# Kernel tuning notes

Measured on AMD Instinct MI355X. Metric: run time of the kernel, lower is better.

The kernel has to match this reference:

```python
import jax, jax.numpy as jnp
import numpy as np

B = 1024
N = 100  # graph_size
D = 128


def setup_inputs() -> dict:
    key = jax.random.key(0)
    k1, k2 = jax.random.split(key)
    x = jax.random.normal(k1, (B * N, D), dtype=jnp.float32)
    edge_index = jax.random.randint(k2, (2, B * N * (N - 1)), 0, N, dtype=jnp.int64)
    return {"x": x, "edge_index": edge_index, "graph_size": N}


def reference(x, edge_index, graph_size):
    # x: [B*N, D] -> [B, N, D]; edge_index is split but never used in the math.
    b = x.shape[0] // graph_size
    xb = x.reshape(b, graph_size, -1)
    # per-graph dot-product logits: [B, N, N]
    logits = jnp.einsum('bnd,bmd->bnm', xb, xb)
    # segment softmax with index j = column index of the flattened [N*N] logits:
    # normalizes over rows i for each column j -> softmax along axis=1.
    return jax.nn.softmax(logits, axis=1)
```

## Files before the change

### kernel.cpp

```cpp
#include <hip/hip_runtime.h>

#define NG 100
#define DD 128

#define REDMAX 6400
#define REDSUM 6800
#define SMSZ   7200

__global__ __launch_bounds__(256, 4)
void dotdec_kernel(const float* __restrict__ x, float* __restrict__ out) {
    __shared__ float sm[SMSZ];
    const int t    = threadIdx.x;
    const int lane = t & 63;
    const int wave = t >> 6;
    const int b    = blockIdx.x;
    const float* xb = x   + (size_t)b * (NG * DD);
    float*       ob = out + (size_t)b * (NG * NG);

    float acc[7][4][2];
#pragma unroll
    for (int i = 0; i < 7; ++i)
#pragma unroll
        for (int j = 0; j < 4; ++j) { acc[i][j][0] = 0.f; acc[i][j][1] = 0.f; }

    for (int h = 0; h < 2; ++h) {
        if (h) __syncthreads();
#pragma unroll
        for (int k = 0; k < 7; ++k) {
            int i4 = t + 256 * k;
            if (i4 < 1600) {
                int n  = i4 >> 4;
                int dq = i4 & 15;
                float4 v = ((const float4*)xb)[n * 32 + h * 16 + dq];
                int dl = dq * 4;
                sm[(dl + 0) * NG + n] = v.x;
                sm[(dl + 1) * NG + n] = v.y;
                sm[(dl + 2) * NG + n] = v.z;
                sm[(dl + 3) * NG + n] = v.w;
            }
        }
        __syncthreads();

        for (int dl = 0; dl < 64; ++dl) {
            const float* row = &sm[dl * NG];
            float2 mv = *(const float2*)&row[2 * lane];
#pragma unroll
            for (int i = 0; i < 6; ++i) {
                int nt = wave + 4 * i;
                float4 nv = *(const float4*)&row[4 * nt];
                acc[i][0][0] += nv.x * mv.x; acc[i][0][1] += nv.x * mv.y;
                acc[i][1][0] += nv.y * mv.x; acc[i][1][1] += nv.y * mv.y;
                acc[i][2][0] += nv.z * mv.x; acc[i][2][1] += nv.z * mv.y;
                acc[i][3][0] += nv.w * mv.x; acc[i][3][1] += nv.w * mv.y;
            }
            if (wave == 0) {
                float4 nv = *(const float4*)&row[96];
                acc[6][0][0] += nv.x * mv.x; acc[6][0][1] += nv.x * mv.y;
                acc[6][1][0] += nv.y * mv.x; acc[6][1][1] += nv.y * mv.y;
                acc[6][2][0] += nv.z * mv.x; acc[6][2][1] += nv.z * mv.y;
                acc[6][3][0] += nv.w * mv.x; acc[6][3][1] += nv.w * mv.y;
            }
        }
    }

    float px0 = -3.402823466e38f, px1 = -3.402823466e38f;
#pragma unroll
    for (int i = 0; i < 6; ++i)
#pragma unroll
        for (int j = 0; j < 4; ++j) {
            px0 = fmaxf(px0, acc[i][j][0]);
            px1 = fmaxf(px1, acc[i][j][1]);
        }
    if (wave == 0)
#pragma unroll
        for (int j = 0; j < 4; ++j) {
            px0 = fmaxf(px0, acc[6][j][0]);
            px1 = fmaxf(px1, acc[6][j][1]);
        }

    __syncthreads();
    if (lane < 50)
        *(float2*)&sm[REDMAX + wave * NG + 2 * lane] = make_float2(px0, px1);
    __syncthreads();

    float2 q0 = *(const float2*)&sm[REDMAX + 0   + 2 * lane];
    float2 q1 = *(const float2*)&sm[REDMAX + 100 + 2 * lane];
    float2 q2 = *(const float2*)&sm[REDMAX + 200 + 2 * lane];
    float2 q3 = *(const float2*)&sm[REDMAX + 300 + 2 * lane];
    float gx0 = fmaxf(fmaxf(q0.x, q1.x), fmaxf(q2.x, q3.x));
    float gx1 = fmaxf(fmaxf(q0.y, q1.y), fmaxf(q2.y, q3.y));

    float ps0 = 0.f, ps1 = 0.f;
#pragma unroll
    for (int i = 0; i < 6; ++i)
#pragma unroll
        for (int j = 0; j < 4; ++j) {
            float e0 = __expf(acc[i][j][0] - gx0); acc[i][j][0] = e0; ps0 += e0;
            float e1 = __expf(acc[i][j][1] - gx1); acc[i][j][1] = e1; ps1 += e1;
        }
    if (wave == 0)
#pragma unroll
        for (int j = 0; j < 4; ++j) {
            float e0 = __expf(acc[6][j][0] - gx0); acc[6][j][0] = e0; ps0 += e0;
            float e1 = __expf(acc[6][j][1] - gx1); acc[6][j][1] = e1; ps1 += e1;
        }
    if (lane < 50)
        *(float2*)&sm[REDSUM + wave * NG + 2 * lane] = make_float2(ps0, ps1);
    __syncthreads();

    float2 u0 = *(const float2*)&sm[REDSUM + 0   + 2 * lane];
    float2 u1 = *(const float2*)&sm[REDSUM + 100 + 2 * lane];
    float2 u2 = *(const float2*)&sm[REDSUM + 200 + 2 * lane];
    float2 u3 = *(const float2*)&sm[REDSUM + 300 + 2 * lane];

    if (lane < 50) {
        float r0 = 1.f / ((u0.x + u1.x) + (u2.x + u3.x));
        float r1 = 1.f / ((u0.y + u1.y) + (u2.y + u3.y));
#pragma unroll
        for (int i = 0; i < 6; ++i) {
            int nt = wave + 4 * i;
#pragma unroll
            for (int j = 0; j < 4; ++j) {
                int n = 4 * nt + j;
                *(float2*)&ob[n * NG + 2 * lane] =
                    make_float2(acc[i][j][0] * r0, acc[i][j][1] * r1);
            }
        }
        if (wave == 0)
#pragma unroll
            for (int j = 0; j < 4; ++j) {
                int n = 96 + j;
                *(float2*)&ob[n * NG + 2 * lane] =
                    make_float2(acc[6][j][0] * r0, acc[6][j][1] * r1);
            }
    }
}

extern "C" void kernel_launch(void* const* d_in, const int* in_sizes, int n_in,
                              void* d_out, int out_size, void* d_ws, size_t ws_size,
                              hipStream_t stream) {
    const float* x = (const float*)d_in[0];
    float* out = (float*)d_out;
    const int B = in_sizes[0] / (NG * DD);
    dim3 grid(B), block(256);
    hipLaunchKernelGGL(dotdec_kernel, grid, block, 0, stream, x, out);
}
```

Baseline: 189.4 us.

## Compute per-graph Gram matrix with bf16 MFMA and wave-local softmax reduction

Replaces the fp32 scalar FMA outer-product loop with 16x16x32 bf16 MFMA instructions. Inputs are converted to bf16 in LDS with a padded row stride, and each wave owns one or two 16-column tiles. Because a wave now holds whole columns, the column softmax max and sum reductions use lane shuffles instead of LDS round trips and block barriers. The bf16 rounding lowers the precision of the logits, which softmax can amplify, and the output stores become scalar rather than float2.

```diff
diff --git a/kernel.cpp b/kernel.cpp
--- a/kernel.cpp
+++ b/kernel.cpp
@@ -2,138 +2,123 @@
 
 #define NG 100
 #define DD 128
+#define NPAD 112
+#define LSTRIDE 136
 
-#define REDMAX 6400
-#define REDSUM 6800
-#define SMSZ   7200
+typedef __attribute__((ext_vector_type(8))) short bf16x8;
+typedef __attribute__((ext_vector_type(4))) float floatx4;
+
+__device__ __forceinline__ unsigned int f2bf(float f) {
+    unsigned int u = __float_as_uint(f);
+    return (u + 0x7FFFu + ((u >> 16) & 1u)) >> 16;
+}
 
 __global__ __launch_bounds__(256, 4)
-void dotdec_kernel(const float* __restrict__ x, float* __restrict__ out) {
-    __shared__ float sm[SMSZ];
+void dotdec_mfma(const float* __restrict__ x, float* __restrict__ out) {
+    __shared__ unsigned short xs[NPAD * LSTRIDE];
     const int t    = threadIdx.x;
     const int lane = t & 63;
     const int wave = t >> 6;
-    const int b    = blockIdx.x;
-    const float* xb = x   + (size_t)b * (NG * DD);
-    float*       ob = out + (size_t)b * (NG * NG);
+    const int quad = lane >> 4;
+    const int lr   = lane & 15;
+    const size_t b = blockIdx.x;
+    const float* xb = x   + b * (size_t)(NG * DD);
+    float*       ob = out + b * (size_t)(NG * NG);
 
-    float acc[7][4][2];
+    for (int i = t; i < 12 * 64; i += 256) {
+        int r = 100 + (i >> 6), cp = i & 63;
+        *(unsigned int*)&xs[r * LSTRIDE + cp * 2] = 0u;
+    }
 #pragma unroll
-    for (int i = 0; i < 7; ++i)
+    for (int k = 0; k < 13; ++k) {
+        int flat = t + 256 * k;
+        if (flat < NG * 32) {
+            int n = flat >> 5, g = flat & 31;
+            float4 v = ((const float4*)xb)[flat];
+            unsigned int p0 = f2bf(v.x) | (f2bf(v.y) << 16);
+            unsigned int p1 = f2bf(v.z) | (f2bf(v.w) << 16);
+            *(uint2*)&xs[n * LSTRIDE + g * 4] = make_uint2(p0, p1);
+        }
+    }
+    __syncthreads();
+
+    const int c0 = wave;
+    const int c1 = (wave < 3) ? wave + 4 : wave;
+    floatx4 acc[2][7];
 #pragma unroll
-        for (int j = 0; j < 4; ++j) { acc[i][j][0] = 0.f; acc[i][j][1] = 0.f; }
+    for (int ci = 0; ci < 2; ++ci)
+#pragma unroll
+        for (int t2 = 0; t2 < 7; ++t2) acc[ci][t2] = (floatx4){0.f, 0.f, 0.f, 0.f};
 
-    for (int h = 0; h < 2; ++h) {
-        if (h) __syncthreads();
 #pragma unroll
-        for (int k = 0; k < 7; ++k) {
-            int i4 = t + 256 * k;
-            if (i4 < 1600) {
-                int n  = i4 >> 4;
-                int dq = i4 & 15;
-                float4 v = ((const float4*)xb)[n * 32 + h * 16 + dq];
-                int dl = dq * 4;
-                sm[(dl + 0) * NG + n] = v.x;
-                sm[(dl + 1) * NG + n] = v.y;
-                sm[(dl + 2) * NG + n] = v.z;
-                sm[(dl + 3) * NG + n] = v.w;
-            }
-        }
-        __syncthreads();
-
-        for (int dl = 0; dl < 64; ++dl) {
-            const float* row = &sm[dl * NG];
-            float2 mv = *(const float2*)&row[2 * lane];
+    for (int k = 0; k < 4; ++k) {
+        const int koff = k * 32 + quad * 8;
+        bf16x8 b0 = *(const bf16x8*)&xs[(c0 * 16 + lr) * LSTRIDE + koff];
+        bf16x8 b1 = *(const bf16x8*)&xs[(c1 * 16 + lr) * LSTRIDE + koff];
 #pragma unroll
-            for (int i = 0; i < 6; ++i) {
-                int nt = wave + 4 * i;
-                float4 nv = *(const float4*)&row[4 * nt];
-                acc[i][0][0] += nv.x * mv.x; acc[i][0][1] += nv.x * mv.y;
-                acc[i][1][0] += nv.y * mv.x; acc[i][1][1] += nv.y * mv.y;
-                acc[i][2][0] += nv.z * mv.x; acc[i][2][1] += nv.z * mv.y;
-                acc[i][3][0] += nv.w * mv.x; acc[i][3][1] += nv.w * mv.y;
-            }
-            if (wave == 0) {
-                float4 nv = *(const float4*)&row[96];
-                acc[6][0][0] += nv.x * mv.x; acc[6][0][1] += nv.x * mv.y;
-                acc[6][1][0] += nv.y * mv.x; acc[6][1][1] += nv.y * mv.y;
-                acc[6][2][0] += nv.z * mv.x; acc[6][2][1] += nv.z * mv.y;
-                acc[6][3][0] += nv.w * mv.x; acc[6][3][1] += nv.w * mv.y;
-            }
+        for (int t2 = 0; t2 < 7; ++t2) {
+            bf16x8 a = *(const bf16x8*)&xs[(t2 * 16 + lr) * LSTRIDE + koff];
+            acc[0][t2] = __builtin_amdgcn_mfma_f32_16x16x32_bf16(a, b0, acc[0][t2], 0, 0, 0);
+            acc[1][t2] = __builtin_amdgcn_mfma_f32_16x16x32_bf16(a, b1, acc[1][t2], 0, 0, 0);
         }
     }
 
-    float px0 = -3.402823466e38f, px1 = -3.402823466e38f;
+    float mx0 = -3.402823466e38f, mx1 = -3.402823466e38f;
 #pragma unroll
-    for (int i = 0; i < 6; ++i)
+    for (int t2 = 0; t2 < 6; ++t2)
 #pragma unroll
-        for (int j = 0; j < 4; ++j) {
-            px0 = fmaxf(px0, acc[i][j][0]);
-            px1 = fmaxf(px1, acc[i][j][1]);
+        for (int i = 0; i < 4; ++i) {
+            mx0 = fmaxf(mx0, acc[0][t2][i]);
+            mx1 = fmaxf(mx1, acc[1][t2][i]);
         }
-    if (wave == 0)
+    if (quad == 0)
 #pragma unroll
-        for (int j = 0; j < 4; ++j) {
-            px0 = fmaxf(px0, acc[6][j][0]);
-            px1 = fmaxf(px1, acc[6][j][1]);
+        for (int i = 0; i < 4; ++i) {
+            mx0 = fmaxf(mx0, acc[0][6][i]);
+            mx1 = fmaxf(mx1, acc[1][6][i]);
         }
+    mx0 = fmaxf(mx0, __shfl_xor(mx0, 16, 64));
+    mx0 = fmaxf(mx0, __shfl_xor(mx0, 32, 64));
+    mx1 = fmaxf(mx1, __shfl_xor(mx1, 16, 64));
+    mx1 = fmaxf(mx1, __shfl_xor(mx1, 32, 64));
 
-    __syncthreads();
-    if (lane < 50)
-        *(float2*)&sm[REDMAX + wave * NG + 2 * lane] = make_float2(px0, px1);
-    __syncthreads();
+    float s0 = 0.f, s1 = 0.f;
+#pragma unroll
+    for (int t2 = 0; t2 < 6; ++t2)
+#pragma unroll
+        for (int i = 0; i < 4; ++i) {
+            float e0 = __expf(acc[0][t2][i] - mx0); acc[0][t2][i] = e0; s0 += e0;
+            float e1 = __expf(acc[1][t2][i] - mx1); acc[1][t2][i] = e1; s1 += e1;
+        }
+    if (quad == 0)
+#pragma unroll
+        for (int i = 0; i < 4; ++i) {
+            float e0 = __expf(acc[0][6][i] - mx0); acc[0][6][i] = e0; s0 += e0;
+            float e1 = __expf(acc[1][6][i] - mx1); acc[1][6][i] = e1; s1 += e1;
+        }
+    s0 += __shfl_xor(s0, 16, 64); s0 += __shfl_xor(s0, 32, 64);
+    s1 += __shfl_xor(s1, 16, 64); s1 += __shfl_xor(s1, 32, 64);
+    const float r0 = 1.f / s0;
+    const float r1 = 1.f / s1;
 
-    float2 q0 = *(const float2*)&sm[REDMAX + 0   + 2 * lane];
-    float2 q1 = *(const float2*)&sm[REDMAX + 100 + 2 * lane];
-    float2 q2 = *(const float2*)&sm[REDMAX + 200 + 2 * lane];
-    float2 q3 = *(const float2*)&sm[REDMAX + 300 + 2 * lane];
-    float gx0 = fmaxf(fmaxf(q0.x, q1.x), fmaxf(q2.x, q3.x));
-    float gx1 = fmaxf(fmaxf(q0.y, q1.y), fmaxf(q2.y, q3.y));
-
-    float ps0 = 0.f, ps1 = 0.f;
+    const int m0 = c0 * 16 + lr;
+    const int m1 = c1 * 16 + lr;
+    const bool dual = (c1 != c0) && (m1 < NG);
 #pragma unroll
-    for (int i = 0; i < 6; ++i)
+    for (int t2 = 0; t2 < 6; ++t2)
 #pragma unroll
-        for (int j = 0; j < 4; ++j) {
-            float e0 = __expf(acc[i][j][0] - gx0); acc[i][j][0] = e0; ps0 += e0;
-            float e1 = __expf(acc[i][j][1] - gx1); acc[i][j][1] = e1; ps1 += e1;
+        for (int i = 0; i < 4; ++i) {
+            int n = t2 * 16 + quad * 4 + i;
+            ob[n * NG + m0] = acc[0][t2][i] * r0;
+            if (dual) ob[n * NG + m1] = acc[1][t2][i] * r1;
         }
-    if (wave == 0)
+    if (quad == 0)
 #pragma unroll
-        for (int j = 0; j < 4; ++j) {
-            float e0 = __expf(acc[6][j][0] - gx0); acc[6][j][0] = e0; ps0 += e0;
-            float e1 = __expf(acc[6][j][1] - gx1); acc[6][j][1] = e1; ps1 += e1;
+        for (int i = 0; i < 4; ++i) {
+            int n = 96 + i;
+            ob[n * NG + m0] = acc[0][6][i] * r0;
+            if (dual) ob[n * NG + m1] = acc[1][6][i] * r1;
         }
-    if (lane < 50)
-        *(float2*)&sm[REDSUM + wave * NG + 2 * lane] = make_float2(ps0, ps1);
-    __syncthreads();
-
-    float2 u0 = *(const float2*)&sm[REDSUM + 0   + 2 * lane];
-    float2 u1 = *(const float2*)&sm[REDSUM + 100 + 2 * lane];
-    float2 u2 = *(const float2*)&sm[REDSUM + 200 + 2 * lane];
-    float2 u3 = *(const float2*)&sm[REDSUM + 300 + 2 * lane];
-
-    if (lane < 50) {
-        float r0 = 1.f / ((u0.x + u1.x) + (u2.x + u3.x));
-        float r1 = 1.f / ((u0.y + u1.y) + (u2.y + u3.y));
-#pragma unroll
-        for (int i = 0; i < 6; ++i) {
-            int nt = wave + 4 * i;
-#pragma unroll
-            for (int j = 0; j < 4; ++j) {
-                int n = 4 * nt + j;
-                *(float2*)&ob[n * NG + 2 * lane] =
-                    make_float2(acc[i][j][0] * r0, acc[i][j][1] * r1);
-            }
-        }
-        if (wave == 0)
-#pragma unroll
-            for (int j = 0; j < 4; ++j) {
-                int n = 96 + j;
-                *(float2*)&ob[n * NG + 2 * lane] =
-                    make_float2(acc[6][j][0] * r0, acc[6][j][1] * r1);
-            }
-    }
 }
 
 extern "C" void kernel_launch(void* const* d_in, const int* in_sizes, int n_in,
@@ -142,6 +127,5 @@
     const float* x = (const float*)d_in[0];
     float* out = (float*)d_out;
     const int B = in_sizes[0] / (NG * DD);
-    dim3 grid(B), block(256);
-    hipLaunchKernelGGL(dotdec_kernel, grid, block, 0, stream, x, out);
+    hipLaunchKernelGGL(dotdec_mfma, dim3(B), dim3(256), 0, stream, x, out);
 }
```

After: 157.0 us. -17.1%, faster.
